# Kernel tuning notes

Measured on AMD Instinct MI355X. Metric: run time of the kernel, lower is better.

## Reference

```python
import jax, jax.numpy as jnp
import numpy as np

EPS = 1e-12  # torch F.normalize clamp_min eps


def _agnn_conv(x, src, dst, beta, n):
    # x: [N, D]; src/dst: [E] (message flows src -> dst, softmax over dst's in-edges)
    xn = x / jnp.maximum(jnp.linalg.norm(x, axis=-1, keepdims=True), EPS)
    alpha = beta[0] * jnp.sum(xn[src] * xn[dst], axis=-1)            # [E] cosine sim * beta
    amax = jax.ops.segment_max(alpha, dst, num_segments=n)           # stable segment softmax
    ex = jnp.exp(alpha - amax[dst])
    denom = jax.ops.segment_sum(ex, dst, num_segments=n)
    w = ex / denom[dst]                                              # [E]
    return jax.ops.segment_sum(x[src] * w[:, None], dst, num_segments=n)


def setup_inputs() -> dict:
    key = jax.random.key(0)
    ks = jax.random.split(key, 8)
    N, E, G = 131072, 4194304, 2048
    x = jax.random.normal(ks[0], (N, 75), dtype=jnp.float32)
    edge_index = jax.random.randint(ks[1], (2, E), 0, N, dtype=jnp.int64)
    batch = jnp.sort(jax.random.randint(ks[2], (N,), 0, G, dtype=jnp.int64))
    lin1_w = jax.random.normal(ks[3], (16, 75), dtype=jnp.float32) * (1.0 / np.sqrt(75))
    lin1_b = jnp.zeros((16,), jnp.float32)
    beta1 = jnp.ones((1,), jnp.float32)   # prop1: requires_grad=False, beta=1
    beta2 = jnp.ones((1,), jnp.float32)   # prop2: learnable beta, init 1
    lin2_w = jax.random.normal(ks[4], (64, 16), dtype=jnp.float32) * (1.0 / np.sqrt(16))
    lin2_b = jnp.zeros((64,), jnp.float32)
    gather_w = jax.random.normal(ks[5], (1, 64), dtype=jnp.float32) * (1.0 / np.sqrt(64))
    gather_b = jnp.zeros((1,), jnp.float32)
    return {"x": x, "edge_index": edge_index, "batch": batch, "num_graphs": G,
            "lin1_w": lin1_w, "lin1_b": lin1_b, "beta1": beta1, "beta2": beta2,
            "lin2_w": lin2_w, "lin2_b": lin2_b, "gather_w": gather_w, "gather_b": gather_b}


def reference(x, edge_index, batch, num_graphs, lin1_w, lin1_b, beta1, beta2,
              lin2_w, lin2_b, gather_w, gather_b):
    n = x.shape[0]
    # PyG AGNNConv adds self-loops by default
    loops = jnp.arange(n, dtype=edge_index.dtype)
    src = jnp.concatenate([edge_index[0], loops])
    dst = jnp.concatenate([edge_index[1], loops])
    # dropout is identity in eval mode
    h = jax.nn.relu(x @ lin1_w.T + lin1_b)          # [N, 16]
    h = _agnn_conv(h, src, dst, beta1, n)
    h = _agnn_conv(h, src, dst, beta2, n)
    h = h @ lin2_w.T + lin2_b                        # [N, 64]
    y = jax.ops.segment_sum(h, batch, num_segments=num_graphs)  # global_add_pool [G, 64]
    return y @ gather_w.T + gather_b                 # [G, 1]
```

## Files before the change

### kernel.cpp

```cpp
#include <hip/hip_runtime.h>
#include <hip/hip_bf16.h>
#include <hip/hip_fp16.h>
#include <math.h>

#define SSEPS 1e-24f
#define NPB 256
#define NPB_SHIFT 8
#define SRC_BITS 17
#define SRC_MASK ((1 << SRC_BITS) - 1)
#define NB 512
#define CAP_B 8832
#define SC_EDGES 8192
#define SCB 512
#define SC_T 512
#define CSR_T 512
#define DBINS 256

union QRowU2 { int4 v; _Float16 h[8]; };



__global__ void init_gcursor(int* g, int* hist) {
    int i = threadIdx.x;
    if (i < NB) g[i] = i * CAP_B;
    if (i < DBINS) hist[i] = 0;
}

__global__ void init_out(float* out, const float* gb, int G) {
    int g = blockIdx.x * blockDim.x + threadIdx.x;
    if (g < G) out[g] = gb[0];
}

__global__ void compute_v(const float* l2w, const float* l2b, const float* gw,
                          float* vbuf) {
    int t = threadIdx.x;
    if (t < 16) {
        float a = 0.f;
        for (int j = 0; j < 64; ++j) a = fmaf(gw[j], l2w[j * 16 + t], a);
        vbuf[t] = a;
    } else if (t == 16) {
        float a = 0.f;
        for (int j = 0; j < 64; ++j) a = fmaf(gw[j], l2b[j], a);
        vbuf[16] = a;
    }
}

__global__ void lin1_relu(const float* __restrict__ x,
                          const float* __restrict__ W1,
                          const float* __restrict__ b1,
                          int* __restrict__ rec1, int N, int D) {
    __shared__ float Ws[16 * 75];
    __shared__ float Bs[16];
    for (int i = threadIdx.x; i < 16 * D; i += blockDim.x) Ws[i] = W1[i];
    if (threadIdx.x < 16) Bs[threadIdx.x] = b1[threadIdx.x];
    __syncthreads();

    int node = blockIdx.x * (blockDim.x >> 4) + (threadIdx.x >> 4);
    int c = threadIdx.x & 15;
    if (node >= N) return;

    const float* xr = x + (size_t)node * D;
    float acc = Bs[c];
    for (int k = 0; k < D; ++k) acc = fmaf(xr[k], Ws[c * D + k], acc);
    float h = fmaxf(acc, 0.f);

    float hn = __shfl_xor(h, 1);
    if (!(c & 1)) {
        union { _Float16 hh[2]; int i; } u;
        u.hh[0] = (_Float16)h;
        u.hh[1] = (_Float16)hn;
        rec1[8 * node + (c >> 1)] = u.i;
    }
}


__global__ __launch_bounds__(SC_T) void bucket_scatter(
    const int* __restrict__ src, const int* __restrict__ dst,
    int E, int* __restrict__ gcursor, int* __restrict__ packed) {
    __shared__ int lout[SC_EDGES];
    __shared__ int h[SCB];
    __shared__ int s[SCB];
    __shared__ int delta[SCB];
    int t = threadIdx.x;
    int base = blockIdx.x * SC_EDGES;
    int cnt = E - base;
    if (cnt > SC_EDGES) cnt = SC_EDGES;

    if (t < SCB) h[t] = 0;
    __syncthreads();
    for (int i = t; i < cnt; i += SC_T)
        atomicAdd(&h[dst[base + i] >> NPB_SHIFT], 1);
    __syncthreads();
    if (t < SCB) s[t] = h[t];
    __syncthreads();
    for (int off = 1; off < SCB; off <<= 1) {
        int a = (t < SCB && t >= off) ? s[t - off] : 0;
        __syncthreads();
        if (t < SCB) s[t] += a;
        __syncthreads();
    }
    if (t < SCB) {
        int c = h[t];
        int ex = s[t] - c;
        int gp = c ? atomicAdd(&gcursor[t], c) : 0;
        delta[t] = gp - ex;
        h[t] = ex;
    }
    __syncthreads();
    for (int i = t; i < cnt; i += SC_T) {
        int d = dst[base + i];
        int b = d >> NPB_SHIFT;
        int pos = atomicAdd(&h[b], 1);
        lout[pos] = ((d & (NPB - 1)) << SRC_BITS) | src[base + i];
    }
    __syncthreads();
    for (int i = t; i < cnt; i += SC_T) {
        int lo = 0, hi = SCB - 1;
        while (lo < hi) {
            int mid = (lo + hi) >> 1;
            if (s[mid] > i) hi = mid;
            else lo = mid + 1;
        }
        packed[delta[lo] + i] = lout[i];
    }
}

__global__ __launch_bounds__(CSR_T) void csr_build(
    const int* __restrict__ packed, const int* __restrict__ gcursor,
    int* __restrict__ deg, int* __restrict__ offs,
    int* __restrict__ csr_src, int* __restrict__ hist, int N) {
    __shared__ int lout[CAP_B];
    __shared__ int ldeg[NPB];
    __shared__ int lofs[NPB];
    __shared__ int lhist[DBINS];
    int b = blockIdx.x;
    int t = threadIdx.x;
    int e0 = b * CAP_B;
    int cnt = gcursor[b] - e0;
    if (t < NPB) ldeg[t] = 0;
    if (t < DBINS) lhist[t] = 0;
    __syncthreads();
    for (int i = t; i < cnt; i += CSR_T)
        atomicAdd(&ldeg[packed[e0 + i] >> SRC_BITS], 1);
    __syncthreads();
    int v = (t < NPB) ? ldeg[t] : 0;
    if (t < NPB) lofs[t] = v;
    if (t < NPB) atomicAdd(&lhist[v < DBINS ? v : DBINS - 1], 1);
    __syncthreads();
    for (int off = 1; off < NPB; off <<= 1) {
        int u = (t < NPB && t >= off) ? lofs[t - off] : 0;
        __syncthreads();
        if (t < NPB) lofs[t] += u;
        __syncthreads();
    }
    if (t < NPB) {
        int ex = lofs[t] - v;
        int node = (b << NPB_SHIFT) + t;
        if (node < N) {
            deg[node] = v;
            offs[node] = e0 + ex;
        }
        lofs[t] = ex;
    }
    __syncthreads();
    for (int i = t; i < cnt; i += CSR_T) {
        int p = packed[e0 + i];
        int pos = atomicAdd(&lofs[p >> SRC_BITS], 1);
        lout[pos] = p & SRC_MASK;
    }
    __syncthreads();
    for (int i = t; i < cnt; i += CSR_T)
        csr_src[e0 + i] = lout[i];
    if (t < DBINS && lhist[t]) atomicAdd(&hist[t], lhist[t]);
}

__global__ void deg_scan(const int* __restrict__ hist, int* __restrict__ cursor) {
    __shared__ int s[DBINS];
    int t = threadIdx.x;
    int h = hist[t];
    s[t] = h;
    __syncthreads();
    for (int off = 1; off < DBINS; off <<= 1) {
        int a = (t >= off) ? s[t - off] : 0;
        __syncthreads();
        s[t] += a;
        __syncthreads();
    }
    cursor[t] = s[t] - h;
}

__global__ void deg_scatter(const int* __restrict__ deg, const int* __restrict__ offs,
                            int* __restrict__ cursor, int* __restrict__ perm,
                            int* __restrict__ sdeg, int* __restrict__ soffs, int N) {
    __shared__ int lh[DBINS];
    __shared__ int lb[DBINS];
    int t = threadIdx.x;
    if (t < DBINS) lh[t] = 0;
    __syncthreads();
    int i = blockIdx.x * blockDim.x + t;
    int bin = 0, r = 0, dv = 0;
    if (i < N) {
        dv = deg[i];
        bin = dv < DBINS ? dv : DBINS - 1;
        r = atomicAdd(&lh[bin], 1);
    }
    __syncthreads();
    if (t < DBINS && lh[t]) lb[t] = atomicAdd(&cursor[t], lh[t]);
    __syncthreads();
    if (i < N) {
        int p = lb[bin] + r;
        perm[p] = i;
        sdeg[p] = dv;
        soffs[p] = offs[i];
    }
}

__global__ __launch_bounds__(256) void agnn_conv1(
    const int* __restrict__ rec1,
    const int* __restrict__ soffs, const int* __restrict__ sdeg,
    const int* __restrict__ csr, const int* __restrict__ perm,
    const float* __restrict__ beta_p,
    int* __restrict__ rec2, int N) {
    int tid = blockIdx.x * blockDim.x + threadIdx.x;
    int slot = tid >> 1;
    int q = tid & 1;
    if (slot >= N) return;
    int node = perm[slot];
    float beta = beta_p[0];
    const int4* rp = (const int4*)rec1;

    QRowU2 rdu;
    rdu.v = rp[2 * node + q];
    float xd[8];
#pragma unroll
    for (int k = 0; k < 8; ++k) xd[k] = (float)rdu.h[k];

    float ssd = 0.f;
#pragma unroll
    for (int k = 0; k < 8; ++k) ssd = fmaf(xd[k], xd[k], ssd);
    ssd += __shfl_xor(ssd, 1);
    float invsd = rsqrtf(fmaxf(ssd, SSEPS));

    float e0 = __expf(beta * ssd * invsd * invsd);
    float denom = e0;
    float acc[8];
#pragma unroll
    for (int k = 0; k < 8; ++k) acc[k] = e0 * xd[k];

    int start = soffs[slot], cnt = sdeg[slot];
    int i = 0;
    for (; i + 8 <= cnt; i += 8) {
        int j[8];
        QRowU2 r[8];
#pragma unroll
        for (int u = 0; u < 8; ++u) j[u] = __builtin_nontemporal_load(&csr[start + i + u]);
#pragma unroll
        for (int u = 0; u < 8; ++u) r[u].v = rp[2 * j[u] + q];
#pragma unroll
        for (int u = 0; u < 8; ++u) {
            float d = 0.f, ss = 0.f;
            float hs[8];
#pragma unroll
            for (int k = 0; k < 8; ++k) {
                hs[k] = (float)r[u].h[k];
                d = fmaf(xd[k], hs[k], d);
                ss = fmaf(hs[k], hs[k], ss);
            }
            d += __shfl_xor(d, 1);
            ss += __shfl_xor(ss, 1);
            float ee = __expf(beta * d * invsd * rsqrtf(fmaxf(ss, SSEPS)));
            denom += ee;
#pragma unroll
            for (int k = 0; k < 8; ++k) acc[k] = fmaf(ee, hs[k], acc[k]);
        }
    }
    for (; i < cnt; ++i) {
        int j = __builtin_nontemporal_load(&csr[start + i]);
        QRowU2 r;
        r.v = rp[2 * j + q];
        float d = 0.f, ss = 0.f;
        float hs[8];
#pragma unroll
        for (int k = 0; k < 8; ++k) {
            hs[k] = (float)r.h[k];
            d = fmaf(xd[k], hs[k], d);
            ss = fmaf(hs[k], hs[k], ss);
        }
        d += __shfl_xor(d, 1);
        ss += __shfl_xor(ss, 1);
        float ee = __expf(beta * d * invsd * rsqrtf(fmaxf(ss, SSEPS)));
        denom += ee;
#pragma unroll
        for (int k = 0; k < 8; ++k) acc[k] = fmaf(ee, hs[k], acc[k]);
    }

    float inv = 1.f / denom;
    QRowU2 w;
#pragma unroll
    for (int k = 0; k < 8; ++k) w.h[k] = (_Float16)(acc[k] * inv);
    ((int4*)rec2)[2 * node + q] = w.v;
}

__global__ __launch_bounds__(256) void agnn_conv2(
    const int* __restrict__ rec2,
    const int* __restrict__ soffs, const int* __restrict__ sdeg,
    const int* __restrict__ csr, const int* __restrict__ perm,
    const float* __restrict__ beta_p,
    const float* __restrict__ vbuf,
    float* __restrict__ rbuf, int N) {
    int tid = blockIdx.x * blockDim.x + threadIdx.x;
    int slot = tid >> 1;
    int q = tid & 1;
    if (slot >= N) return;
    int node = perm[slot];
    float beta = beta_p[0];
    const int4* rp = (const int4*)rec2;

    float vq[8];
#pragma unroll
    for (int k = 0; k < 8; ++k) vq[k] = vbuf[8 * q + k];

    QRowU2 rdu;
    rdu.v = rp[2 * node + q];
    float xd[8];
#pragma unroll
    for (int k = 0; k < 8; ++k) xd[k] = (float)rdu.h[k];

    float ssd = 0.f, pd = 0.f;
#pragma unroll
    for (int k = 0; k < 8; ++k) {
        ssd = fmaf(xd[k], xd[k], ssd);
        pd = fmaf(vq[k], xd[k], pd);
    }
    ssd += __shfl_xor(ssd, 1);
    pd += __shfl_xor(pd, 1);
    float invsd = rsqrtf(fmaxf(ssd, SSEPS));

    float e0 = __expf(beta * ssd * invsd * invsd);
    float denom = e0;
    float acc = e0 * pd;

    int start = soffs[slot], cnt = sdeg[slot];
    int i = 0;
    for (; i + 8 <= cnt; i += 8) {
        int j[8];
        QRowU2 r[8];
#pragma unroll
        for (int u = 0; u < 8; ++u) j[u] = __builtin_nontemporal_load(&csr[start + i + u]);
#pragma unroll
        for (int u = 0; u < 8; ++u) r[u].v = rp[2 * j[u] + q];
#pragma unroll
        for (int u = 0; u < 8; ++u) {
            float d = 0.f, ss = 0.f, pv = 0.f;
#pragma unroll
            for (int k = 0; k < 8; ++k) {
                float hs = (float)r[u].h[k];
                d = fmaf(xd[k], hs, d);
                ss = fmaf(hs, hs, ss);
                pv = fmaf(vq[k], hs, pv);
            }
            d += __shfl_xor(d, 1);
            ss += __shfl_xor(ss, 1);
            pv += __shfl_xor(pv, 1);
            float ee = __expf(beta * d * invsd * rsqrtf(fmaxf(ss, SSEPS)));
            denom += ee;
            acc = fmaf(ee, pv, acc);
        }
    }
    for (; i < cnt; ++i) {
        int j = __builtin_nontemporal_load(&csr[start + i]);
        QRowU2 r;
        r.v = rp[2 * j + q];
        float d = 0.f, ss = 0.f, pv = 0.f;
#pragma unroll
        for (int k = 0; k < 8; ++k) {
            float hs = (float)r.h[k];
            d = fmaf(xd[k], hs, d);
            ss = fmaf(hs, hs, ss);
            pv = fmaf(vq[k], hs, pv);
        }
        d += __shfl_xor(d, 1);
        ss += __shfl_xor(ss, 1);
        pv += __shfl_xor(pv, 1);
        float ee = __expf(beta * d * invsd * rsqrtf(fmaxf(ss, SSEPS)));
        denom += ee;
        acc = fmaf(ee, pv, acc);
    }
    if (q == 0) rbuf[node] = acc / denom;
}

__global__ void pool_kernel(const float* __restrict__ r, const int* __restrict__ batch,
                            const float* __restrict__ vbuf, float* __restrict__ out,
                            int N) {
    int base = (blockIdx.x * blockDim.x + threadIdx.x) * 8;
    if (base >= N) return;
    float c0 = vbuf[16];
    int lim = base + 8;
    if (lim > N) lim = N;
    float run = 0.f;
    int g = -1;
    for (int i = base; i < lim; ++i) {
        int gi = batch[i];
        if (gi != g) {
            if (g >= 0) atomicAdd(&out[g], run);
            g = gi;
            run = 0.f;
        }
        run += r[i] + c0;
    }
    if (g >= 0) atomicAdd(&out[g], run);
}


extern "C" void kernel_launch(void* const* d_in, const int* in_sizes, int n_in,
                              void* d_out, int out_size, void* d_ws, size_t ws_size,
                              hipStream_t stream) {
    const float* x = (const float*)d_in[0];
    const int* edge_index = (const int*)d_in[1];
    const int* batch = (const int*)d_in[2];
    const float* lin1_w = (const float*)d_in[4];
    const float* lin1_b = (const float*)d_in[5];
    const float* beta1 = (const float*)d_in[6];
    const float* beta2 = (const float*)d_in[7];
    const float* lin2_w = (const float*)d_in[8];
    const float* lin2_b = (const float*)d_in[9];
    const float* gather_w = (const float*)d_in[10];
    const float* gather_b = (const float*)d_in[11];
    float* out = (float*)d_out;

    const int N = in_sizes[2];
    const int E = in_sizes[1] / 2;
    const int D = in_sizes[0] / N;
    const int G = out_size;

    const int* src = edge_index;
    const int* dst = edge_index + E;

    float* w = (float*)d_ws;
    int* rec1 = (int*)w;                 w += (size_t)N * 8;
    int* rec2 = (int*)w;                 w += (size_t)N * 8;
    float* rbuf = w;                     w += N;
    float* vbuf = w;                     w += 32;
    int* deg = (int*)w;                  w += N;
    int* offs = (int*)w;                 w += N;
    int* packed = (int*)w;               w += (size_t)NB * CAP_B;
    int* csr_src = (int*)w;              w += (size_t)NB * CAP_B;
    int* gcursor = (int*)w;              w += NB;
    int* perm = (int*)w;                 w += N;
    int* sdeg = (int*)w;                 w += N;
    int* soffs = (int*)w;                w += N;
    int* hist = (int*)w;                 w += DBINS;
    int* cursor = (int*)w;               w += DBINS;

    const int B = 256;
    dim3 gridNode16((N + (B / 16) - 1) / (B / 16));
    dim3 gridNode2((2 * N + B - 1) / B);

    init_gcursor<<<dim3(1), NB, 0, stream>>>(gcursor, hist);
    bucket_scatter<<<dim3((E + SC_EDGES - 1) / SC_EDGES), SC_T, 0, stream>>>(
        src, dst, E, gcursor, packed);
    csr_build<<<dim3(NB), CSR_T, 0, stream>>>(packed, gcursor, deg, offs, csr_src,
                                              hist, N);

    deg_scan<<<dim3(1), DBINS, 0, stream>>>(hist, cursor);
    deg_scatter<<<dim3((N + B - 1) / B), B, 0, stream>>>(deg, offs, cursor, perm,
                                                         sdeg, soffs, N);

    lin1_relu<<<gridNode16, B, 0, stream>>>(x, lin1_w, lin1_b, rec1, N, D);
    compute_v<<<dim3(1), 64, 0, stream>>>(lin2_w, lin2_b, gather_w, vbuf);

    agnn_conv1<<<gridNode2, B, 0, stream>>>(rec1, soffs, sdeg, csr_src, perm,
                                            beta1, rec2, N);
    agnn_conv2<<<gridNode2, B, 0, stream>>>(rec2, soffs, sdeg, csr_src, perm,
                                            beta2, vbuf, rbuf, N);

    init_out<<<dim3((G + B - 1) / B), B, 0, stream>>>(out, gather_b, G);
    pool_kernel<<<dim3((N / 8 + B - 1) / B), B, 0, stream>>>(rbuf, batch, vbuf, out, N);
}
```

Measured before the change: 318.7 us.

## Fuse setup kernels into one megakernel and drop degree-sorted node permutation

Merges the edge bucket scatter, lin1+ReLU, the lin2/gather vector precompute and output init into a single launch that dispatches work by block index, and replaces the init kernel with a memset. It removes the degree histogram, scan and scatter kernels, so the conv kernels process nodes in natural order rather than degree-sorted order. The scatter now writes destination indices into shared memory, which avoids the per-edge binary search, and the chunk size is halved. The cost is that degree-sorted load balancing is gone, so warps may diverge more on uneven degrees.

```diff
diff --git a/kernel.cpp b/kernel.cpp
--- a/kernel.cpp
+++ b/kernel.cpp
@@ -10,142 +10,123 @@
 #define SRC_MASK ((1 << SRC_BITS) - 1)
 #define NB 512
 #define CAP_B 8832
-#define SC_EDGES 8192
+#define SC_EDGES 4096
 #define SCB 512
-#define SC_T 512
+#define MG_T 512
+#define MG_SCAT 1024
+#define MG_LIN 4096
 #define CSR_T 512
-#define DBINS 256
 
 union QRowU2 { int4 v; _Float16 h[8]; };
 
 
-
-__global__ void init_gcursor(int* g, int* hist) {
-    int i = threadIdx.x;
-    if (i < NB) g[i] = i * CAP_B;
-    if (i < DBINS) hist[i] = 0;
-}
-
-__global__ void init_out(float* out, const float* gb, int G) {
-    int g = blockIdx.x * blockDim.x + threadIdx.x;
-    if (g < G) out[g] = gb[0];
-}
-
-__global__ void compute_v(const float* l2w, const float* l2b, const float* gw,
-                          float* vbuf) {
+__global__ __launch_bounds__(MG_T) void mega1(
+    const int* __restrict__ src, const int* __restrict__ dst, int E,
+    int* __restrict__ gcursor, int* __restrict__ packed,
+    const float* __restrict__ x, const float* __restrict__ W1,
+    const float* __restrict__ b1, int* __restrict__ rec1, int N, int D,
+    const float* __restrict__ l2w, const float* __restrict__ l2b,
+    const float* __restrict__ gw, float* __restrict__ vbuf,
+    float* __restrict__ out, const float* __restrict__ gb, int G) {
+    __shared__ int sh[2 * SC_EDGES + 3 * SCB];
+    int bid = blockIdx.x;
     int t = threadIdx.x;
-    if (t < 16) {
-        float a = 0.f;
-        for (int j = 0; j < 64; ++j) a = fmaf(gw[j], l2w[j * 16 + t], a);
-        vbuf[t] = a;
-    } else if (t == 16) {
-        float a = 0.f;
-        for (int j = 0; j < 64; ++j) a = fmaf(gw[j], l2b[j], a);
-        vbuf[16] = a;
-    }
-}
-
-__global__ void lin1_relu(const float* __restrict__ x,
-                          const float* __restrict__ W1,
-                          const float* __restrict__ b1,
-                          int* __restrict__ rec1, int N, int D) {
-    __shared__ float Ws[16 * 75];
-    __shared__ float Bs[16];
-    for (int i = threadIdx.x; i < 16 * D; i += blockDim.x) Ws[i] = W1[i];
-    if (threadIdx.x < 16) Bs[threadIdx.x] = b1[threadIdx.x];
-    __syncthreads();
-
-    int node = blockIdx.x * (blockDim.x >> 4) + (threadIdx.x >> 4);
-    int c = threadIdx.x & 15;
-    if (node >= N) return;
-
-    const float* xr = x + (size_t)node * D;
-    float acc = Bs[c];
-    for (int k = 0; k < D; ++k) acc = fmaf(xr[k], Ws[c * D + k], acc);
-    float h = fmaxf(acc, 0.f);
-
-    float hn = __shfl_xor(h, 1);
-    if (!(c & 1)) {
-        union { _Float16 hh[2]; int i; } u;
-        u.hh[0] = (_Float16)h;
-        u.hh[1] = (_Float16)hn;
-        rec1[8 * node + (c >> 1)] = u.i;
-    }
-}
-
-
-__global__ __launch_bounds__(SC_T) void bucket_scatter(
-    const int* __restrict__ src, const int* __restrict__ dst,
-    int E, int* __restrict__ gcursor, int* __restrict__ packed) {
-    __shared__ int lout[SC_EDGES];
-    __shared__ int h[SCB];
-    __shared__ int s[SCB];
-    __shared__ int delta[SCB];
-    int t = threadIdx.x;
-    int base = blockIdx.x * SC_EDGES;
-    int cnt = E - base;
-    if (cnt > SC_EDGES) cnt = SC_EDGES;
-
-    if (t < SCB) h[t] = 0;
-    __syncthreads();
-    for (int i = t; i < cnt; i += SC_T)
-        atomicAdd(&h[dst[base + i] >> NPB_SHIFT], 1);
-    __syncthreads();
-    if (t < SCB) s[t] = h[t];
-    __syncthreads();
-    for (int off = 1; off < SCB; off <<= 1) {
-        int a = (t < SCB && t >= off) ? s[t - off] : 0;
-        __syncthreads();
-        if (t < SCB) s[t] += a;
-        __syncthreads();
-    }
-    if (t < SCB) {
-        int c = h[t];
-        int ex = s[t] - c;
-        int gp = c ? atomicAdd(&gcursor[t], c) : 0;
-        delta[t] = gp - ex;
-        h[t] = ex;
-    }
-    __syncthreads();
-    for (int i = t; i < cnt; i += SC_T) {
-        int d = dst[base + i];
-        int b = d >> NPB_SHIFT;
-        int pos = atomicAdd(&h[b], 1);
-        lout[pos] = ((d & (NPB - 1)) << SRC_BITS) | src[base + i];
-    }
-    __syncthreads();
-    for (int i = t; i < cnt; i += SC_T) {
-        int lo = 0, hi = SCB - 1;
-        while (lo < hi) {
-            int mid = (lo + hi) >> 1;
-            if (s[mid] > i) hi = mid;
-            else lo = mid + 1;
-        }
-        packed[delta[lo] + i] = lout[i];
+
+    if (bid < MG_SCAT) {
+        int* lout = sh;
+        int* loutd = sh + SC_EDGES;
+        int* h = sh + 2 * SC_EDGES;
+        int* s = h + SCB;
+        int* delta = s + SCB;
+        int base = bid * SC_EDGES;
+        int cnt = E - base;
+        if (cnt > SC_EDGES) cnt = SC_EDGES;
+
+        h[t] = 0;
+        __syncthreads();
+        for (int i = t; i < cnt; i += MG_T)
+            atomicAdd(&h[dst[base + i] >> NPB_SHIFT], 1);
+        __syncthreads();
+        s[t] = h[t];
+        __syncthreads();
+        for (int off = 1; off < SCB; off <<= 1) {
+            int a = (t >= off) ? s[t - off] : 0;
+            __syncthreads();
+            s[t] += a;
+            __syncthreads();
+        }
+        {
+            int c = h[t];
+            int ex = s[t] - c;
+            int gp = c ? atomicAdd(&gcursor[t], c) : 0;
+            delta[t] = (t * CAP_B + gp) - ex;
+            h[t] = ex;
+        }
+        __syncthreads();
+        for (int i = t; i < cnt; i += MG_T) {
+            int d = dst[base + i];
+            int b = d >> NPB_SHIFT;
+            int pos = atomicAdd(&h[b], 1);
+            lout[pos] = ((d & (NPB - 1)) << SRC_BITS) | src[base + i];
+            loutd[pos] = delta[b] + pos;
+        }
+        __syncthreads();
+        for (int i = t; i < cnt; i += MG_T)
+            packed[loutd[i]] = lout[i];
+    } else if (bid < MG_SCAT + MG_LIN) {
+        float* Ws = (float*)sh;
+        float* Bs = Ws + 16 * 75;
+        for (int i = t; i < 16 * D; i += MG_T) Ws[i] = W1[i];
+        if (t < 16) Bs[t] = b1[t];
+        __syncthreads();
+        int node = (bid - MG_SCAT) * (MG_T >> 4) + (t >> 4);
+        int c = t & 15;
+        if (node >= N) return;
+        const float* xr = x + (size_t)node * D;
+        float acc = Bs[c];
+        for (int k = 0; k < D; ++k) acc = fmaf(xr[k], Ws[c * D + k], acc);
+        float hv = fmaxf(acc, 0.f);
+        float hn = __shfl_xor(hv, 1);
+        if (!(c & 1)) {
+            union { _Float16 hh[2]; int i; } u;
+            u.hh[0] = (_Float16)hv;
+            u.hh[1] = (_Float16)hn;
+            rec1[8 * node + (c >> 1)] = u.i;
+        }
+    } else if (bid == MG_SCAT + MG_LIN) {
+        if (t < 16) {
+            float a = 0.f;
+            for (int j = 0; j < 64; ++j) a = fmaf(gw[j], l2w[j * 16 + t], a);
+            vbuf[t] = a;
+        } else if (t == 16) {
+            float a = 0.f;
+            for (int j = 0; j < 64; ++j) a = fmaf(gw[j], l2b[j], a);
+            vbuf[16] = a;
+        }
+    } else {
+        int g = (bid - (MG_SCAT + MG_LIN + 1)) * MG_T + t;
+        if (g < G) out[g] = gb[0];
     }
 }
 
 __global__ __launch_bounds__(CSR_T) void csr_build(
     const int* __restrict__ packed, const int* __restrict__ gcursor,
     int* __restrict__ deg, int* __restrict__ offs,
-    int* __restrict__ csr_src, int* __restrict__ hist, int N) {
+    int* __restrict__ csr_src, int N) {
     __shared__ int lout[CAP_B];
     __shared__ int ldeg[NPB];
     __shared__ int lofs[NPB];
-    __shared__ int lhist[DBINS];
     int b = blockIdx.x;
     int t = threadIdx.x;
     int e0 = b * CAP_B;
-    int cnt = gcursor[b] - e0;
+    int cnt = gcursor[b];
     if (t < NPB) ldeg[t] = 0;
-    if (t < DBINS) lhist[t] = 0;
     __syncthreads();
     for (int i = t; i < cnt; i += CSR_T)
         atomicAdd(&ldeg[packed[e0 + i] >> SRC_BITS], 1);
     __syncthreads();
     int v = (t < NPB) ? ldeg[t] : 0;
     if (t < NPB) lofs[t] = v;
-    if (t < NPB) atomicAdd(&lhist[v < DBINS ? v : DBINS - 1], 1);
     __syncthreads();
     for (int off = 1; off < NPB; off <<= 1) {
         int u = (t < NPB && t >= off) ? lofs[t - off] : 0;
@@ -171,61 +152,17 @@
     __syncthreads();
     for (int i = t; i < cnt; i += CSR_T)
         csr_src[e0 + i] = lout[i];
-    if (t < DBINS && lhist[t]) atomicAdd(&hist[t], lhist[t]);
-}
-
-__global__ void deg_scan(const int* __restrict__ hist, int* __restrict__ cursor) {
-    __shared__ int s[DBINS];
-    int t = threadIdx.x;
-    int h = hist[t];
-    s[t] = h;
-    __syncthreads();
-    for (int off = 1; off < DBINS; off <<= 1) {
-        int a = (t >= off) ? s[t - off] : 0;
-        __syncthreads();
-        s[t] += a;
-        __syncthreads();
-    }
-    cursor[t] = s[t] - h;
-}
-
-__global__ void deg_scatter(const int* __restrict__ deg, const int* __restrict__ offs,
-                            int* __restrict__ cursor, int* __restrict__ perm,
-                            int* __restrict__ sdeg, int* __restrict__ soffs, int N) {
-    __shared__ int lh[DBINS];
-    __shared__ int lb[DBINS];
-    int t = threadIdx.x;
-    if (t < DBINS) lh[t] = 0;
-    __syncthreads();
-    int i = blockIdx.x * blockDim.x + t;
-    int bin = 0, r = 0, dv = 0;
-    if (i < N) {
-        dv = deg[i];
-        bin = dv < DBINS ? dv : DBINS - 1;
-        r = atomicAdd(&lh[bin], 1);
-    }
-    __syncthreads();
-    if (t < DBINS && lh[t]) lb[t] = atomicAdd(&cursor[t], lh[t]);
-    __syncthreads();
-    if (i < N) {
-        int p = lb[bin] + r;
-        perm[p] = i;
-        sdeg[p] = dv;
-        soffs[p] = offs[i];
-    }
 }
 
 __global__ __launch_bounds__(256) void agnn_conv1(
     const int* __restrict__ rec1,
-    const int* __restrict__ soffs, const int* __restrict__ sdeg,
-    const int* __restrict__ csr, const int* __restrict__ perm,
-    const float* __restrict__ beta_p,
+    const int* __restrict__ offs, const int* __restrict__ deg,
+    const int* __restrict__ csr, const float* __restrict__ beta_p,
     int* __restrict__ rec2, int N) {
     int tid = blockIdx.x * blockDim.x + threadIdx.x;
-    int slot = tid >> 1;
+    int node = tid >> 1;
     int q = tid & 1;
-    if (slot >= N) return;
-    int node = perm[slot];
+    if (node >= N) return;
     float beta = beta_p[0];
     const int4* rp = (const int4*)rec1;
 
@@ -247,7 +184,7 @@
 #pragma unroll
     for (int k = 0; k < 8; ++k) acc[k] = e0 * xd[k];
 
-    int start = soffs[slot], cnt = sdeg[slot];
+    int start = offs[node], cnt = deg[node];
     int i = 0;
     for (; i + 8 <= cnt; i += 8) {
         int j[8];
@@ -303,16 +240,14 @@
 
 __global__ __launch_bounds__(256) void agnn_conv2(
     const int* __restrict__ rec2,
-    const int* __restrict__ soffs, const int* __restrict__ sdeg,
-    const int* __restrict__ csr, const int* __restrict__ perm,
-    const float* __restrict__ beta_p,
+    const int* __restrict__ offs, const int* __restrict__ deg,
+    const int* __restrict__ csr, const float* __restrict__ beta_p,
     const float* __restrict__ vbuf,
     float* __restrict__ rbuf, int N) {
     int tid = blockIdx.x * blockDim.x + threadIdx.x;
-    int slot = tid >> 1;
+    int node = tid >> 1;
     int q = tid & 1;
-    if (slot >= N) return;
-    int node = perm[slot];
+    if (node >= N) return;
     float beta = beta_p[0];
     const int4* rp = (const int4*)rec2;
 
@@ -340,7 +275,7 @@
     float denom = e0;
     float acc = e0 * pd;
 
-    int start = soffs[slot], cnt = sdeg[slot];
+    int start = offs[node], cnt = deg[node];
     int i = 0;
     for (; i + 8 <= cnt; i += 8) {
         int j[8];
@@ -446,34 +381,28 @@
     int* packed = (int*)w;               w += (size_t)NB * CAP_B;
     int* csr_src = (int*)w;              w += (size_t)NB * CAP_B;
     int* gcursor = (int*)w;              w += NB;
-    int* perm = (int*)w;                 w += N;
-    int* sdeg = (int*)w;                 w += N;
-    int* soffs = (int*)w;                w += N;
-    int* hist = (int*)w;                 w += DBINS;
-    int* cursor = (int*)w;               w += DBINS;
 
     const int B = 256;
-    dim3 gridNode16((N + (B / 16) - 1) / (B / 16));
     dim3 gridNode2((2 * N + B - 1) / B);
 
-    init_gcursor<<<dim3(1), NB, 0, stream>>>(gcursor, hist);
-    bucket_scatter<<<dim3((E + SC_EDGES - 1) / SC_EDGES), SC_T, 0, stream>>>(
-        src, dst, E, gcursor, packed);
-    csr_build<<<dim3(NB), CSR_T, 0, stream>>>(packed, gcursor, deg, offs, csr_src,
-                                              hist, N);
-
-    deg_scan<<<dim3(1), DBINS, 0, stream>>>(hist, cursor);
-    deg_scatter<<<dim3((N + B - 1) / B), B, 0, stream>>>(deg, offs, cursor, perm,
-                                                         sdeg, soffs, N);
-
-    lin1_relu<<<gridNode16, B, 0, stream>>>(x, lin1_w, lin1_b, rec1, N, D);
-    compute_v<<<dim3(1), 64, 0, stream>>>(lin2_w, lin2_b, gather_w, vbuf);
-
-    agnn_conv1<<<gridNode2, B, 0, stream>>>(rec1, soffs, sdeg, csr_src, perm,
+    hipMemsetAsync(gcursor, 0, NB * sizeof(int), stream);
+
+    int nScat = (E + SC_EDGES - 1) / SC_EDGES;
+    int nLin = (N + (MG_T / 16) - 1) / (MG_T / 16);
+    int nOut = (G + MG_T - 1) / MG_T;
+    dim3 megaGrid(nScat + nLin + 1 + nOut);
+    mega1<<<megaGrid, MG_T, 0, stream>>>(src, dst, E, gcursor, packed,
+                                         x, lin1_w, lin1_b, rec1, N, D,
+                                         lin2_w, lin2_b, gather_w, vbuf,
+                                         out, gather_b, G);
+
+    csr_build<<<dim3(NB), CSR_T, 0, stream>>>(packed, gcursor, deg, offs,
+                                              csr_src, N);
+
+    agnn_conv1<<<gridNode2, B, 0, stream>>>(rec1, offs, deg, csr_src,
                                             beta1, rec2, N);
-    agnn_conv2<<<gridNode2, B, 0, stream>>>(rec2, soffs, sdeg, csr_src, perm,
+    agnn_conv2<<<gridNode2, B, 0, stream>>>(rec2, offs, deg, csr_src,
                                             beta2, vbuf, rbuf, N);
 
-    init_out<<<dim3((G + B - 1) / B), B, 0, stream>>>(out, gather_b, G);
     pool_kernel<<<dim3((N / 8 + B - 1) / B), B, 0, stream>>>(rbuf, batch, vbuf, out, N);
 }
```

Result: faster. 282.2 us (-11.5%).
